# Performance work log

Measured on AMD Instinct MI355X. Metric: run time of the kernel, lower is better.

Reference implementation:

```python
import jax, jax.numpy as jnp
import numpy as np

HIDDEN = 256
INPUT = 256
OUTPUT = 256
BATCH = 256
SEQ = 512


def setup_inputs() -> dict:
    key = jax.random.key(0)
    ks = jax.random.split(key, 9)
    d = INPUT + HIDDEN
    s = 0.05
    return {
        "x": jax.random.normal(ks[0], (BATCH, SEQ, INPUT), dtype=jnp.float32),
        "Wr": jax.random.normal(ks[1], (d, HIDDEN), dtype=jnp.float32) * s,
        "br": jax.random.normal(ks[2], (HIDDEN,), dtype=jnp.float32) * s,
        "Wz": jax.random.normal(ks[3], (d, HIDDEN), dtype=jnp.float32) * s,
        "bz": jax.random.normal(ks[4], (HIDDEN,), dtype=jnp.float32) * s,
        "Wh": jax.random.normal(ks[5], (d, HIDDEN), dtype=jnp.float32) * s,
        "bh": jax.random.normal(ks[6], (HIDDEN,), dtype=jnp.float32) * s,
        "Wo": jax.random.normal(ks[7], (HIDDEN, OUTPUT), dtype=jnp.float32) * s,
        "bo": jax.random.normal(ks[8], (OUTPUT,), dtype=jnp.float32) * s,
    }


def reference(x, Wr, br, Wz, bz, Wh, bh, Wo, bo):
    # x: [B, S, I]. Sequential GRU cell; only last-step output is returned
    # (the torch loop overwrites `output` each iteration).
    B = x.shape[0]
    h0 = jnp.zeros((B, HIDDEN), dtype=x.dtype)

    def step(h, xt):
        combined = jnp.concatenate([xt, h], axis=1)          # [B, I+H]
        r = jax.nn.sigmoid(combined @ Wr + br)                # reset gate
        z = jax.nn.sigmoid(combined @ Wz + bz)                # update gate
        combined2 = jnp.concatenate([xt, r * h], axis=1)
        h_cand = jnp.tanh(combined2 @ Wh + bh)
        h_new = z * h + (1.0 - z) * h_cand
        return h_new, None

    xs = jnp.swapaxes(x, 0, 1)  # [S, B, I] for scan over time
    h_last, _ = jax.lax.scan(step, h0, xs)
    return h_last @ Wo + bo
```

## Files before the change

### kernel.cpp

```cpp
#include <hip/hip_runtime.h>
#include <math.h>


#define BATCH  256
#define SEQ    512
#define INPUT  256
#define HIDDEN 256
#define DTOT   512
#define NTC    48
#define NT_O   16
#define LOG2E  1.44269504088896f

typedef float          f32x4 __attribute__((ext_vector_type(4)));
typedef short          s16x8 __attribute__((ext_vector_type(8)));
typedef unsigned short u16x8 __attribute__((ext_vector_type(8)));
typedef unsigned int   u32x2 __attribute__((ext_vector_type(2)));

#define WH_OFF   0u
#define WX_OFF   393216u
#define WO_OFF   786432u
#define X_OFF    917504u
#define WS_NEED     (917504ull + 201326592ull)
#define WS_NEED_OLD 786432ull

__device__ __forceinline__ unsigned short f2bf(float f) {
    unsigned int u = __float_as_uint(f);
    u += 0x7FFFu + ((u >> 16) & 1u);
    return (unsigned short)(u >> 16);
}
__device__ __forceinline__ unsigned short f2bf_fast(float f) {
    return (unsigned short)((__float_as_uint(f) + 0x8000u) >> 16);
}
__device__ __forceinline__ float bf2f(unsigned short u) {
    return __uint_as_float(((unsigned int)u) << 16);
}
__device__ __forceinline__ f32x4 cvt4(u32x2 u) {
    f32x4 a;
    a[0] = __uint_as_float(u[0] << 16);
    a[1] = __uint_as_float(u[0] & 0xffff0000u);
    a[2] = __uint_as_float(u[1] << 16);
    a[3] = __uint_as_float(u[1] & 0xffff0000u);
    return a;
}
__device__ __forceinline__ unsigned int pk2bf(float a, float b) {
    return ((__float_as_uint(a) + 0x8000u) >> 16) |
           ((__float_as_uint(b) + 0x8000u) & 0xFFFF0000u);
}
#if __has_builtin(__builtin_amdgcn_exp2f)
#define EXP2F(x) __builtin_amdgcn_exp2f(x)
#else
#define EXP2F(x) exp2f(x)
#endif
#if __has_builtin(__builtin_amdgcn_rcpf)
#define RCPF(x) __builtin_amdgcn_rcpf(x)
#else
#define RCPF(x) (1.0f / (x))
#endif

#define WAITCNT_VM3()   asm volatile("s_waitcnt vmcnt(3)" ::: "memory")
#define WAITCNT_VM4()   asm volatile("s_waitcnt vmcnt(4)" ::: "memory")
#define WAITCNT_LGKM0() asm volatile("s_waitcnt lgkmcnt(0)" ::: "memory")
#define BAR() do { __builtin_amdgcn_s_barrier(); __builtin_amdgcn_sched_barrier(0); } while (0)

__device__ __forceinline__ void async_ld16(const void* g, void* l) {
    __builtin_amdgcn_global_load_lds(
        (const __attribute__((address_space(1))) unsigned int*)g,
        (__attribute__((address_space(3))) unsigned int*)l, 16, 0, 0);
}

__device__ __forceinline__ void ntc_decode(int ntc, int& gate, int& colbase) {
    int w = ntc / 6, s = ntc - 6 * w;
    gate = s >> 1;
    colbase = (2 * w + (s & 1)) * 16;
}

__global__ __launch_bounds__(256) void pack_weights_k(
    const float* __restrict__ Wr, const float* __restrict__ Wz,
    const float* __restrict__ Wh, const float* __restrict__ Wo,
    unsigned short* __restrict__ ws)
{
    int tid = blockIdx.x * 256 + threadIdx.x;
    int tile = tid >> 6;
    int l = tid & 63, quad = l >> 4, lan = l & 15;
    u16x8 v;
    unsigned short* dst;
    if (tile < 768) {
        int isH = tile < 384;
        int t2 = isH ? tile : tile - 384;
        int ntc = t2 >> 3, kt = t2 & 7;
        int gate, colbase;
        ntc_decode(ntc, gate, colbase);
        const float* W = gate == 0 ? Wr : (gate == 1 ? Wz : Wh);
        float scale = (gate == 2) ? 2.f * LOG2E : LOG2E;
        int col = colbase + lan;
        int kbase = (isH ? 256 : 0) + kt * 32 + quad * 8;
        #pragma unroll
        for (int j = 0; j < 8; ++j) v[j] = f2bf(W[(kbase + j) * 256 + col] * scale);
        dst = (unsigned short*)((char*)ws + (isH ? WH_OFF : WX_OFF)) + (size_t)(t2 * 64 + l) * 8;
    } else {
        int t2 = tile - 768;
        int kt = t2 / NT_O, nt = t2 % NT_O;
        int col = nt * 16 + lan;
        int kbase = kt * 32 + quad * 8;
        #pragma unroll
        for (int j = 0; j < 8; ++j) v[j] = f2bf(Wo[(kbase + j) * 256 + col]);
        dst = (unsigned short*)((char*)ws + WO_OFF) + (size_t)(t2 * 64 + l) * 8;
    }
    *(u16x8*)dst = v;
}

__global__ __launch_bounds__(512, 2) void xgemm_k(
    const float* __restrict__ x,
    const float* __restrict__ br, const float* __restrict__ bz, const float* __restrict__ bh,
    unsigned short* __restrict__ ws)
{
    __shared__ __align__(16) unsigned short Xbf[16][264];
    const int th = threadIdx.x, wave = th >> 6, l = th & 63, quad = l >> 4, lan = l & 15;
    const s16x8* WX = (const s16x8*)((char*)ws + WX_OFF);
    s16x8 wx[6][8];
    #pragma unroll
    for (int fi = 0; fi < 6; ++fi)
        #pragma unroll
        for (int kt = 0; kt < 8; ++kt)
            wx[fi][kt] = WX[(((size_t)(6 * wave + fi)) * 8 + kt) * 64 + l];
    f32x4 bias4[6];
    #pragma unroll
    for (int fi = 0; fi < 6; ++fi) {
        int gate, colbase;
        ntc_decode(6 * wave + fi, gate, colbase);
        const float* bb = gate == 0 ? br : (gate == 1 ? bz : bh);
        f32x4 bv = *(const f32x4*)&bb[colbase + quad * 4];
        float scale = (gate == 2 ? 2.f * LOG2E : LOG2E);
        bias4[fi][0] = bv[0] * scale; bias4[fi][1] = bv[1] * scale;
        bias4[fi][2] = bv[2] * scale; bias4[fi][3] = bv[3] * scale;
    }
    u32x2* Xout = (u32x2*)((char*)ws + X_OFF);

    f32x4 xs[2];
    {
        int unit = blockIdx.x * 32, t = unit >> 4, gg = unit & 15;
        #pragma unroll
        for (int rr = 0; rr < 2; ++rr)
            xs[rr] = *(const f32x4*)(x + (((size_t)(gg * 16 + 2 * wave + rr)) * SEQ + t) * INPUT + l * 4);
    }
    for (int uu = 0; uu < 32; ++uu) {
        if (uu > 0) BAR();
        #pragma unroll
        for (int rr = 0; rr < 2; ++rr) {
            u32x2 p;
            p[0] = pk2bf(xs[rr][0], xs[rr][1]);
            p[1] = pk2bf(xs[rr][2], xs[rr][3]);
            *(u32x2*)&Xbf[2 * wave + rr][l * 4] = p;
        }
        if (uu + 1 < 32) {
            int unit = blockIdx.x * 32 + uu + 1, t = unit >> 4, gg = unit & 15;
            #pragma unroll
            for (int rr = 0; rr < 2; ++rr)
                xs[rr] = *(const f32x4*)(x + (((size_t)(gg * 16 + 2 * wave + rr)) * SEQ + t) * INPUT + l * 4);
        }
        WAITCNT_LGKM0();
        BAR();
        f32x4 acc[6];
        #pragma unroll
        for (int fi = 0; fi < 6; ++fi) acc[fi] = bias4[fi];
        #pragma unroll
        for (int kt = 0; kt < 8; ++kt) {
            s16x8 a = *(const s16x8*)&Xbf[lan][kt * 32 + quad * 8];
            #pragma unroll
            for (int fi = 0; fi < 6; ++fi)
                acc[fi] = __builtin_amdgcn_mfma_f32_16x16x32_bf16(wx[fi][kt], a, acc[fi], 0, 0, 0);
        }
        size_t unit = (size_t)blockIdx.x * 32 + uu;
        #pragma unroll
        for (int fi = 0; fi < 6; ++fi) {
            u32x2 p;
            p[0] = pk2bf(acc[fi][0], acc[fi][1]);
            p[1] = pk2bf(acc[fi][2], acc[fi][3]);
            Xout[(unit * NTC + 6 * wave + fi) * 64 + l] = p;
        }
    }
}

__global__ __launch_bounds__(512, 2) void gru_rec_k(
    const float* __restrict__ bo,
    unsigned short* __restrict__ ws,
    float* __restrict__ out)
{
    extern __shared__ __align__(16) char smem[];
    unsigned short (*Hb)[264]  = (unsigned short (*)[264])smem;
    unsigned short (*RHb)[264] = (unsigned short (*)[264])(smem + 8448);
    char* Xr = smem + 16896;

    const int th = threadIdx.x, wave = th >> 6, l = th & 63, quad = l >> 4, lan = l & 15;
    const int b = blockIdx.x;
    const s16x8* WH = (const s16x8*)((char*)ws + WH_OFF);
    s16x8 wfr[2][8], wfz[2][8], wfc[2][8];
    #pragma unroll
    for (int i = 0; i < 2; ++i)
        #pragma unroll
        for (int kt = 0; kt < 8; ++kt) {
            wfr[i][kt] = WH[((6 * wave + i) * 8 + kt) * 64 + l];
            wfz[i][kt] = WH[((6 * wave + 2 + i) * 8 + kt) * 64 + l];
            wfc[i][kt] = WH[((6 * wave + 4 + i) * 8 + kt) * 64 + l];
        }
    for (int idx = th; idx < 16 * 264; idx += 512) ((unsigned short*)Hb)[idx] = 0;
    float h[2][4];
    #pragma unroll
    for (int i = 0; i < 2; ++i)
        #pragma unroll
        for (int r = 0; r < 4; ++r) h[i][r] = 0.f;

    const char* Xg = (const char*)ws + X_OFF;
    {
        const char* sb = Xg + (((size_t)b) * NTC + 6 * wave) * 512;
        char* db = Xr + wave * 3072;
        #pragma unroll
        for (int inst = 0; inst < 3; ++inst)
            async_ld16(sb + inst * 1024 + l * 16, db + inst * 1024);
    }
    __syncthreads();

    for (int t = 0; t < SEQ; ++t) {
        int buf = t & 1;
        {
            int t1 = (t + 1 < SEQ) ? t + 1 : t;
            const char* sb = Xg + (((size_t)(t1 * 16 + b)) * NTC + 6 * wave) * 512;
            char* db = Xr + (buf ^ 1) * 24576 + wave * 3072;
            #pragma unroll
            for (int inst = 0; inst < 3; ++inst)
                async_ld16(sb + inst * 1024 + l * 16, db + inst * 1024);
        }
        WAITCNT_VM3();
        const char* Xw = Xr + buf * 24576 + wave * 3072;

        f32x4 ar[2], az[2];
        #pragma unroll
        for (int i = 0; i < 2; ++i) {
            ar[i] = cvt4(*(const u32x2*)(Xw + (size_t)i * 512 + l * 8));
            az[i] = cvt4(*(const u32x2*)(Xw + (size_t)(2 + i) * 512 + l * 8));
        }
        #pragma unroll
        for (int kt = 0; kt < 8; ++kt) {
            s16x8 a = *(const s16x8*)&Hb[lan][kt * 32 + quad * 8];
            #pragma unroll
            for (int i = 0; i < 2; ++i) {
                ar[i] = __builtin_amdgcn_mfma_f32_16x16x32_bf16(wfr[i][kt], a, ar[i], 0, 0, 0);
                az[i] = __builtin_amdgcn_mfma_f32_16x16x32_bf16(wfz[i][kt], a, az[i], 0, 0, 0);
            }
        }
        #pragma unroll
        for (int i = 0; i < 2; ++i) {
            int colb = (2 * wave + i) * 16 + quad * 4;
            float rg0 = RCPF(1.f + EXP2F(-ar[i][0]));
            float rg1 = RCPF(1.f + EXP2F(-ar[i][1]));
            float rg2 = RCPF(1.f + EXP2F(-ar[i][2]));
            float rg3 = RCPF(1.f + EXP2F(-ar[i][3]));
            u32x2 rp;
            rp[0] = pk2bf(rg0 * h[i][0], rg1 * h[i][1]);
            rp[1] = pk2bf(rg2 * h[i][2], rg3 * h[i][3]);
            *(u32x2*)&RHb[lan][colb] = rp;
        }
        WAITCNT_LGKM0();
        BAR();

        float zg[2][4];
        #pragma unroll
        for (int i = 0; i < 2; ++i)
            #pragma unroll
            for (int r = 0; r < 4; ++r)
                zg[i][r] = RCPF(1.f + EXP2F(-az[i][r]));

        f32x4 ac[2];
        #pragma unroll
        for (int i = 0; i < 2; ++i)
            ac[i] = cvt4(*(const u32x2*)(Xw + (size_t)(4 + i) * 512 + l * 8));
        #pragma unroll
        for (int kt = 0; kt < 8; ++kt) {
            s16x8 a = *(const s16x8*)&RHb[lan][kt * 32 + quad * 8];
            #pragma unroll
            for (int i = 0; i < 2; ++i)
                ac[i] = __builtin_amdgcn_mfma_f32_16x16x32_bf16(wfc[i][kt], a, ac[i], 0, 0, 0);
        }
        #pragma unroll
        for (int i = 0; i < 2; ++i) {
            int colb = (2 * wave + i) * 16 + quad * 4;
            #pragma unroll
            for (int r = 0; r < 4; ++r) {
                float e  = EXP2F(ac[i][r]);
                float hc = (e - 1.f) * RCPF(e + 1.f);
                h[i][r] = zg[i][r] * (h[i][r] - hc) + hc;
            }
            u32x2 hp;
            hp[0] = pk2bf(h[i][0], h[i][1]);
            hp[1] = pk2bf(h[i][2], h[i][3]);
            *(u32x2*)&Hb[lan][colb] = hp;
        }
        WAITCNT_LGKM0();
        BAR();
    }

    const s16x8* WO = (const s16x8*)((char*)ws + WO_OFF);
    #pragma unroll
    for (int i = 0; i < 2; ++i) {
        int nt = 2 * wave + i;
        f32x4 acc = *(const f32x4*)&bo[nt * 16 + quad * 4];
        #pragma unroll
        for (int kt = 0; kt < 8; ++kt) {
            s16x8 a = *(const s16x8*)&Hb[lan][kt * 32 + quad * 8];
            acc = __builtin_amdgcn_mfma_f32_16x16x32_bf16(WO[(kt * NT_O + nt) * 64 + l], a, acc, 0, 0, 0);
        }
        *(f32x4*)&out[(size_t)(b * 16 + lan) * 256 + nt * 16 + quad * 4] = acc;
    }
}

__global__ __launch_bounds__(256) void prep_weights_k(
    const float* __restrict__ Wr, const float* __restrict__ Wz,
    const float* __restrict__ Wh, unsigned short* __restrict__ W16)
{
    const int n = DTOT * HIDDEN;
    int idx = blockIdx.x * 256 + threadIdx.x;
    if (idx >= 3 * n) return;
    int m = idx / n;
    int r = idx - m * n;
    const float* src = (m == 0) ? Wr : ((m == 1) ? Wz : Wh);
    W16[idx] = f2bf(src[r]);
}
__device__ __forceinline__ float ldw(const unsigned short* p) { return bf2f(*p); }
__device__ __forceinline__ float ldw(const float* p)          { return *p; }

template <typename WT>
__global__ __launch_bounds__(256) void gru_seq_k(
    const float* __restrict__ x,
    const WT* __restrict__ Wr, const WT* __restrict__ Wz, const WT* __restrict__ Wh,
    const float* __restrict__ br, const float* __restrict__ bz, const float* __restrict__ bh,
    const float* __restrict__ Wo, const float* __restrict__ bo,
    float* __restrict__ out)
{
    const int b = blockIdx.x, j = threadIdx.x;
    __shared__ float xh[DTOT];
    __shared__ float xrh[DTOT];
    xh[INPUT + j] = 0.0f;
    const float brj = br[j], bzj = bz[j], bhj = bh[j];
    const float* xb = x + (size_t)b * SEQ * INPUT;
    const WT* wrj = Wr + j;
    const WT* wzj = Wz + j;
    const WT* whj = Wh + j;
    __syncthreads();
    for (int t = 0; t < SEQ; ++t) {
        float xv = xb[t * INPUT + j];
        xh[j] = xv; xrh[j] = xv;
        __syncthreads();
        float ar = brj, az = bzj;
        #pragma unroll 8
        for (int k = 0; k < DTOT; ++k) {
            float v = xh[k];
            ar += v * ldw(wrj + k * HIDDEN);
            az += v * ldw(wzj + k * HIDDEN);
        }
        float rg = 1.0f / (1.0f + __expf(-ar));
        float zg = 1.0f / (1.0f + __expf(-az));
        float hj = xh[INPUT + j];
        xrh[INPUT + j] = rg * hj;
        __syncthreads();
        float ah = bhj;
        #pragma unroll 8
        for (int k = 0; k < DTOT; ++k) ah += xrh[k] * ldw(whj + k * HIDDEN);
        float hc = tanhf(ah);
        float hn = zg * hj + (1.0f - zg) * hc;
        xh[INPUT + j] = hn;
        __syncthreads();
    }
    float acc = bo[j];
    #pragma unroll 8
    for (int k = 0; k < HIDDEN; ++k) acc += xh[INPUT + k] * Wo[k * HIDDEN + j];
    out[(size_t)b * HIDDEN + j] = acc;
}

extern "C" void kernel_launch(void* const* d_in, const int* in_sizes, int n_in,
                              void* d_out, int out_size, void* d_ws, size_t ws_size,
                              hipStream_t stream) {
    const float* x  = (const float*)d_in[0];
    const float* Wr = (const float*)d_in[1];
    const float* br = (const float*)d_in[2];
    const float* Wz = (const float*)d_in[3];
    const float* bz = (const float*)d_in[4];
    const float* Wh = (const float*)d_in[5];
    const float* bh = (const float*)d_in[6];
    const float* Wo = (const float*)d_in[7];
    const float* bo = (const float*)d_in[8];
    float* out = (float*)d_out;

    if (ws_size >= WS_NEED) {
        unsigned short* ws = (unsigned short*)d_ws;
        (void)hipFuncSetAttribute((const void*)gru_rec_k,
                                  hipFuncAttributeMaxDynamicSharedMemorySize, 66048);
        pack_weights_k<<<224, 256, 0, stream>>>(Wr, Wz, Wh, Wo, ws);
        xgemm_k<<<256, 512, 0, stream>>>(x, br, bz, bh, ws);
        gru_rec_k<<<16, 512, 66048, stream>>>(bo, ws, out);
    } else if (ws_size >= WS_NEED_OLD) {
        unsigned short* W16 = (unsigned short*)d_ws;
        const size_t n = (size_t)DTOT * HIDDEN;
        prep_weights_k<<<(int)((3 * n + 255) / 256), 256, 0, stream>>>(Wr, Wz, Wh, W16);
        gru_seq_k<unsigned short><<<BATCH, 256, 0, stream>>>(
            x, W16, W16 + n, W16 + 2 * n, br, bz, bh, Wo, bo, out);
    } else {
        gru_seq_k<float><<<BATCH, 256, 0, stream>>>(
            x, Wr, Wz, Wh, br, bz, bh, Wo, bo, out);
    }
}
```

Baseline: 1.053 ms.

## Halve recurrence block to four waves, each owning four column tiles

The recurrent GRU kernel now runs 256 threads (4 waves) per block instead of 512, and each wave handles four 16-column tiles of r, z and candidate gates instead of two. Each wave keeps twice as many weight fragments in registers, and the per-step X prefetch per wave doubles to six async loads. The aim is cheaper barriers and more MFMA work per wave between the two per-step syncs. The cost is heavier register pressure (96 s16x8 weight fragments per lane) and fewer waves to hide MFMA and LDS latency.

```diff
diff --git a/kernel.cpp b/kernel.cpp
--- a/kernel.cpp
+++ b/kernel.cpp
@@ -27,9 +27,6 @@
     unsigned int u = __float_as_uint(f);
     u += 0x7FFFu + ((u >> 16) & 1u);
     return (unsigned short)(u >> 16);
-}
-__device__ __forceinline__ unsigned short f2bf_fast(float f) {
-    return (unsigned short)((__float_as_uint(f) + 0x8000u) >> 16);
 }
 __device__ __forceinline__ float bf2f(unsigned short u) {
     return __uint_as_float(((unsigned int)u) << 16);
@@ -57,8 +54,7 @@
 #define RCPF(x) (1.0f / (x))
 #endif
 
-#define WAITCNT_VM3()   asm volatile("s_waitcnt vmcnt(3)" ::: "memory")
-#define WAITCNT_VM4()   asm volatile("s_waitcnt vmcnt(4)" ::: "memory")
+#define WAITCNT_VM6()   asm volatile("s_waitcnt vmcnt(6)" ::: "memory")
 #define WAITCNT_LGKM0() asm volatile("s_waitcnt lgkmcnt(0)" ::: "memory")
 #define BAR() do { __builtin_amdgcn_s_barrier(); __builtin_amdgcn_sched_barrier(0); } while (0)
 
@@ -181,7 +177,7 @@
     }
 }
 
-__global__ __launch_bounds__(512, 2) void gru_rec_k(
+__global__ __launch_bounds__(256, 1) void gru_rec_k(
     const float* __restrict__ bo,
     unsigned short* __restrict__ ws,
     float* __restrict__ out)
@@ -194,28 +190,30 @@
     const int th = threadIdx.x, wave = th >> 6, l = th & 63, quad = l >> 4, lan = l & 15;
     const int b = blockIdx.x;
     const s16x8* WH = (const s16x8*)((char*)ws + WH_OFF);
-    s16x8 wfr[2][8], wfz[2][8], wfc[2][8];
+    s16x8 wfr[4][8], wfz[4][8], wfc[4][8];
     #pragma unroll
-    for (int i = 0; i < 2; ++i)
+    for (int i2 = 0; i2 < 4; ++i2) {
+        int nb = 6 * (2 * wave + (i2 >> 1)) + (i2 & 1);
         #pragma unroll
         for (int kt = 0; kt < 8; ++kt) {
-            wfr[i][kt] = WH[((6 * wave + i) * 8 + kt) * 64 + l];
-            wfz[i][kt] = WH[((6 * wave + 2 + i) * 8 + kt) * 64 + l];
-            wfc[i][kt] = WH[((6 * wave + 4 + i) * 8 + kt) * 64 + l];
-        }
-    for (int idx = th; idx < 16 * 264; idx += 512) ((unsigned short*)Hb)[idx] = 0;
-    float h[2][4];
+            wfr[i2][kt] = WH[((nb)     * 8 + kt) * 64 + l];
+            wfz[i2][kt] = WH[((nb + 2) * 8 + kt) * 64 + l];
+            wfc[i2][kt] = WH[((nb + 4) * 8 + kt) * 64 + l];
+        }
+    }
+    for (int idx = th; idx < 16 * 264; idx += 256) ((unsigned short*)Hb)[idx] = 0;
+    float h[4][4];
     #pragma unroll
-    for (int i = 0; i < 2; ++i)
-        #pragma unroll
-        for (int r = 0; r < 4; ++r) h[i][r] = 0.f;
+    for (int i2 = 0; i2 < 4; ++i2)
+        #pragma unroll
+        for (int r = 0; r < 4; ++r) h[i2][r] = 0.f;
 
     const char* Xg = (const char*)ws + X_OFF;
     {
-        const char* sb = Xg + (((size_t)b) * NTC + 6 * wave) * 512;
-        char* db = Xr + wave * 3072;
-        #pragma unroll
-        for (int inst = 0; inst < 3; ++inst)
+        const char* sb = Xg + (((size_t)b) * NTC + 12 * wave) * 512;
+        char* db = Xr + wave * 6144;
+        #pragma unroll
+        for (int inst = 0; inst < 6; ++inst)
             async_ld16(sb + inst * 1024 + l * 16, db + inst * 1024);
     }
     __syncthreads();
@@ -224,75 +222,78 @@
         int buf = t & 1;
         {
             int t1 = (t + 1 < SEQ) ? t + 1 : t;
-            const char* sb = Xg + (((size_t)(t1 * 16 + b)) * NTC + 6 * wave) * 512;
-            char* db = Xr + (buf ^ 1) * 24576 + wave * 3072;
-            #pragma unroll
-            for (int inst = 0; inst < 3; ++inst)
+            const char* sb = Xg + (((size_t)(t1 * 16 + b)) * NTC + 12 * wave) * 512;
+            char* db = Xr + (buf ^ 1) * 24576 + wave * 6144;
+            #pragma unroll
+            for (int inst = 0; inst < 6; ++inst)
                 async_ld16(sb + inst * 1024 + l * 16, db + inst * 1024);
         }
-        WAITCNT_VM3();
-        const char* Xw = Xr + buf * 24576 + wave * 3072;
-
-        f32x4 ar[2], az[2];
-        #pragma unroll
-        for (int i = 0; i < 2; ++i) {
-            ar[i] = cvt4(*(const u32x2*)(Xw + (size_t)i * 512 + l * 8));
-            az[i] = cvt4(*(const u32x2*)(Xw + (size_t)(2 + i) * 512 + l * 8));
+        WAITCNT_VM6();
+        const char* Xw = Xr + buf * 24576 + wave * 6144;
+
+        f32x4 ar[4], az[4];
+        #pragma unroll
+        for (int i2 = 0; i2 < 4; ++i2) {
+            int kb = 6 * (i2 >> 1) + (i2 & 1);
+            ar[i2] = cvt4(*(const u32x2*)(Xw + (size_t)(kb)     * 512 + l * 8));
+            az[i2] = cvt4(*(const u32x2*)(Xw + (size_t)(kb + 2) * 512 + l * 8));
         }
         #pragma unroll
         for (int kt = 0; kt < 8; ++kt) {
             s16x8 a = *(const s16x8*)&Hb[lan][kt * 32 + quad * 8];
             #pragma unroll
-            for (int i = 0; i < 2; ++i) {
-                ar[i] = __builtin_amdgcn_mfma_f32_16x16x32_bf16(wfr[i][kt], a, ar[i], 0, 0, 0);
-                az[i] = __builtin_amdgcn_mfma_f32_16x16x32_bf16(wfz[i][kt], a, az[i], 0, 0, 0);
+            for (int i2 = 0; i2 < 4; ++i2) {
+                ar[i2] = __builtin_amdgcn_mfma_f32_16x16x32_bf16(wfr[i2][kt], a, ar[i2], 0, 0, 0);
+                az[i2] = __builtin_amdgcn_mfma_f32_16x16x32_bf16(wfz[i2][kt], a, az[i2], 0, 0, 0);
             }
         }
         #pragma unroll
-        for (int i = 0; i < 2; ++i) {
-            int colb = (2 * wave + i) * 16 + quad * 4;
-            float rg0 = RCPF(1.f + EXP2F(-ar[i][0]));
-            float rg1 = RCPF(1.f + EXP2F(-ar[i][1]));
-            float rg2 = RCPF(1.f + EXP2F(-ar[i][2]));
-            float rg3 = RCPF(1.f + EXP2F(-ar[i][3]));
+        for (int i2 = 0; i2 < 4; ++i2) {
+            int colb = (4 * wave + i2) * 16 + quad * 4;
+            float rg0 = RCPF(1.f + EXP2F(-ar[i2][0]));
+            float rg1 = RCPF(1.f + EXP2F(-ar[i2][1]));
+            float rg2 = RCPF(1.f + EXP2F(-ar[i2][2]));
+            float rg3 = RCPF(1.f + EXP2F(-ar[i2][3]));
             u32x2 rp;
-            rp[0] = pk2bf(rg0 * h[i][0], rg1 * h[i][1]);
-            rp[1] = pk2bf(rg2 * h[i][2], rg3 * h[i][3]);
+            rp[0] = pk2bf(rg0 * h[i2][0], rg1 * h[i2][1]);
+            rp[1] = pk2bf(rg2 * h[i2][2], rg3 * h[i2][3]);
             *(u32x2*)&RHb[lan][colb] = rp;
         }
         WAITCNT_LGKM0();
         BAR();
 
-        float zg[2][4];
-        #pragma unroll
-        for (int i = 0; i < 2; ++i)
+        float zg[4][4];
+        #pragma unroll
+        for (int i2 = 0; i2 < 4; ++i2)
             #pragma unroll
             for (int r = 0; r < 4; ++r)
-                zg[i][r] = RCPF(1.f + EXP2F(-az[i][r]));
-
-        f32x4 ac[2];
-        #pragma unroll
-        for (int i = 0; i < 2; ++i)
-            ac[i] = cvt4(*(const u32x2*)(Xw + (size_t)(4 + i) * 512 + l * 8));
+                zg[i2][r] = RCPF(1.f + EXP2F(-az[i2][r]));
+
+        f32x4 ac[4];
+        #pragma unroll
+        for (int i2 = 0; i2 < 4; ++i2) {
+            int kb = 6 * (i2 >> 1) + (i2 & 1);
+            ac[i2] = cvt4(*(const u32x2*)(Xw + (size_t)(kb + 4) * 512 + l * 8));
+        }
         #pragma unroll
         for (int kt = 0; kt < 8; ++kt) {
             s16x8 a = *(const s16x8*)&RHb[lan][kt * 32 + quad * 8];
             #pragma unroll
-            for (int i = 0; i < 2; ++i)
-                ac[i] = __builtin_amdgcn_mfma_f32_16x16x32_bf16(wfc[i][kt], a, ac[i], 0, 0, 0);
-        }
-        #pragma unroll
-        for (int i = 0; i < 2; ++i) {
-            int colb = (2 * wave + i) * 16 + quad * 4;
+            for (int i2 = 0; i2 < 4; ++i2)
+                ac[i2] = __builtin_amdgcn_mfma_f32_16x16x32_bf16(wfc[i2][kt], a, ac[i2], 0, 0, 0);
+        }
+        #pragma unroll
+        for (int i2 = 0; i2 < 4; ++i2) {
+            int colb = (4 * wave + i2) * 16 + quad * 4;
             #pragma unroll
             for (int r = 0; r < 4; ++r) {
-                float e  = EXP2F(ac[i][r]);
+                float e  = EXP2F(ac[i2][r]);
                 float hc = (e - 1.f) * RCPF(e + 1.f);
-                h[i][r] = zg[i][r] * (h[i][r] - hc) + hc;
+                h[i2][r] = zg[i2][r] * (h[i2][r] - hc) + hc;
             }
             u32x2 hp;
-            hp[0] = pk2bf(h[i][0], h[i][1]);
-            hp[1] = pk2bf(h[i][2], h[i][3]);
+            hp[0] = pk2bf(h[i2][0], h[i2][1]);
+            hp[1] = pk2bf(h[i2][2], h[i2][3]);
             *(u32x2*)&Hb[lan][colb] = hp;
         }
         WAITCNT_LGKM0();
@@ -301,8 +302,8 @@
 
     const s16x8* WO = (const s16x8*)((char*)ws + WO_OFF);
     #pragma unroll
-    for (int i = 0; i < 2; ++i) {
-        int nt = 2 * wave + i;
+    for (int i2 = 0; i2 < 4; ++i2) {
+        int nt = 4 * wave + i2;
         f32x4 acc = *(const f32x4*)&bo[nt * 16 + quad * 4];
         #pragma unroll
         for (int kt = 0; kt < 8; ++kt) {
@@ -396,7 +397,7 @@
                                   hipFuncAttributeMaxDynamicSharedMemorySize, 66048);
         pack_weights_k<<<224, 256, 0, stream>>>(Wr, Wz, Wh, Wo, ws);
         xgemm_k<<<256, 512, 0, stream>>>(x, br, bz, bh, ws);
-        gru_rec_k<<<16, 512, 66048, stream>>>(bo, ws, out);
+        gru_rec_k<<<16, 256, 66048, stream>>>(bo, ws, out);
     } else if (ws_size >= WS_NEED_OLD) {
         unsigned short* W16 = (unsigned short*)d_ws;
         const size_t n = (size_t)DTOT * HIDDEN;
```

Measured after the change: 1.421 ms. +34.9%, slower.

## Fuse input GEMM and recurrence into one kernel with flag-based producer/consumer overlap

Applied to the files above, without the earlier changes.

Merges the x-projection GEMM and the sequential GRU recurrence into one launch. 240 producer blocks compute per-timestep input projections and publish per-unit flags with release stores, while 16 consumer blocks spin on those flags and run the recurrence concurrently. This is meant to hide the input GEMM behind the recurrence and remove a kernel boundary. The cost is spin-waiting, reliance on all blocks being co-resident, and a larger workspace for the flags, which pack_weights_k now zeroes.

```diff
diff --git a/kernel.cpp b/kernel.cpp
--- a/kernel.cpp
+++ b/kernel.cpp
@@ -10,6 +10,7 @@
 #define NTC    48
 #define NT_O   16
 #define LOG2E  1.44269504088896f
+#define NPROD  240
 
 typedef float          f32x4 __attribute__((ext_vector_type(4)));
 typedef short          s16x8 __attribute__((ext_vector_type(8)));
@@ -20,16 +21,15 @@
 #define WX_OFF   393216u
 #define WO_OFF   786432u
 #define X_OFF    917504u
-#define WS_NEED     (917504ull + 201326592ull)
-#define WS_NEED_OLD 786432ull
+#define FLAG_OFF (917504u + 201326592u)
+#define WS_NEED_FUSED (917504ull + 201326592ull + 32768ull)
+#define WS_NEED_SPLIT (917504ull + 201326592ull)
+#define WS_NEED_OLD   786432ull
 
 __device__ __forceinline__ unsigned short f2bf(float f) {
     unsigned int u = __float_as_uint(f);
     u += 0x7FFFu + ((u >> 16) & 1u);
     return (unsigned short)(u >> 16);
-}
-__device__ __forceinline__ unsigned short f2bf_fast(float f) {
-    return (unsigned short)((__float_as_uint(f) + 0x8000u) >> 16);
 }
 __device__ __forceinline__ float bf2f(unsigned short u) {
     return __uint_as_float(((unsigned int)u) << 16);
@@ -77,9 +77,13 @@
 __global__ __launch_bounds__(256) void pack_weights_k(
     const float* __restrict__ Wr, const float* __restrict__ Wz,
     const float* __restrict__ Wh, const float* __restrict__ Wo,
-    unsigned short* __restrict__ ws)
+    unsigned short* __restrict__ ws, int zflags)
 {
     int tid = blockIdx.x * 256 + threadIdx.x;
+    if (zflags && tid < 4096) {
+        u32x2 z; z[0] = 0u; z[1] = 0u;
+        ((u32x2*)((char*)ws + FLAG_OFF))[tid] = z;
+    }
     int tile = tid >> 6;
     int l = tid & 63, quad = l >> 4, lan = l & 15;
     u16x8 v;
@@ -109,6 +113,227 @@
     *(u16x8*)dst = v;
 }
 
+__global__ __launch_bounds__(512, 2) void fused_k(
+    const float* __restrict__ x,
+    const float* __restrict__ br, const float* __restrict__ bz, const float* __restrict__ bh,
+    const float* __restrict__ bo,
+    unsigned short* __restrict__ ws,
+    float* __restrict__ out)
+{
+    extern __shared__ __align__(16) char smem[];
+    const int bid = blockIdx.x;
+    const int th = threadIdx.x, wave = th >> 6, l = th & 63, quad = l >> 4, lan = l & 15;
+    int* flags = (int*)((char*)ws + FLAG_OFF);
+
+    if (bid >= 16) {
+        unsigned short (*Xbf)[264] = (unsigned short (*)[264])smem;
+        const int p = bid - 16;
+        const s16x8* WX = (const s16x8*)((char*)ws + WX_OFF);
+        s16x8 wx[6][8];
+        #pragma unroll
+        for (int fi = 0; fi < 6; ++fi)
+            #pragma unroll
+            for (int kt = 0; kt < 8; ++kt)
+                wx[fi][kt] = WX[(((size_t)(6 * wave + fi)) * 8 + kt) * 64 + l];
+        f32x4 bias4[6];
+        #pragma unroll
+        for (int fi = 0; fi < 6; ++fi) {
+            int gate, colbase;
+            ntc_decode(6 * wave + fi, gate, colbase);
+            const float* bb = gate == 0 ? br : (gate == 1 ? bz : bh);
+            f32x4 bv = *(const f32x4*)&bb[colbase + quad * 4];
+            float scale = (gate == 2 ? 2.f * LOG2E : LOG2E);
+            bias4[fi][0] = bv[0] * scale; bias4[fi][1] = bv[1] * scale;
+            bias4[fi][2] = bv[2] * scale; bias4[fi][3] = bv[3] * scale;
+        }
+        u32x2* Xout = (u32x2*)((char*)ws + X_OFF);
+
+        f32x4 xs[2];
+        {
+            int t = p >> 4, gg = p & 15;
+            #pragma unroll
+            for (int rr = 0; rr < 2; ++rr)
+                xs[rr] = *(const f32x4*)(x + (((size_t)(gg * 16 + 2 * wave + rr)) * SEQ + t) * INPUT + l * 4);
+        }
+        for (int uu = p; uu < SEQ * 16; uu += NPROD) {
+            if (uu != p) BAR();
+            #pragma unroll
+            for (int rr = 0; rr < 2; ++rr) {
+                u32x2 pk;
+                pk[0] = pk2bf(xs[rr][0], xs[rr][1]);
+                pk[1] = pk2bf(xs[rr][2], xs[rr][3]);
+                *(u32x2*)&Xbf[2 * wave + rr][l * 4] = pk;
+            }
+            int un = uu + NPROD;
+            if (un < SEQ * 16) {
+                int t = un >> 4, gg = un & 15;
+                #pragma unroll
+                for (int rr = 0; rr < 2; ++rr)
+                    xs[rr] = *(const f32x4*)(x + (((size_t)(gg * 16 + 2 * wave + rr)) * SEQ + t) * INPUT + l * 4);
+            }
+            WAITCNT_LGKM0();
+            BAR();
+            f32x4 acc[6];
+            #pragma unroll
+            for (int fi = 0; fi < 6; ++fi) acc[fi] = bias4[fi];
+            #pragma unroll
+            for (int kt = 0; kt < 8; ++kt) {
+                s16x8 a = *(const s16x8*)&Xbf[lan][kt * 32 + quad * 8];
+                #pragma unroll
+                for (int fi = 0; fi < 6; ++fi)
+                    acc[fi] = __builtin_amdgcn_mfma_f32_16x16x32_bf16(wx[fi][kt], a, acc[fi], 0, 0, 0);
+            }
+            #pragma unroll
+            for (int fi = 0; fi < 6; ++fi) {
+                u32x2 pk;
+                pk[0] = pk2bf(acc[fi][0], acc[fi][1]);
+                pk[1] = pk2bf(acc[fi][2], acc[fi][3]);
+                Xout[((size_t)uu * NTC + 6 * wave + fi) * 64 + l] = pk;
+            }
+            __threadfence();
+            __syncthreads();
+            if (th == 0)
+                __hip_atomic_store(&flags[uu], 1, __ATOMIC_RELEASE, __HIP_MEMORY_SCOPE_AGENT);
+        }
+        return;
+    }
+
+    unsigned short (*Hb)[264]  = (unsigned short (*)[264])smem;
+    unsigned short (*RHb)[264] = (unsigned short (*)[264])(smem + 8448);
+    char* Xr = smem + 16896;
+    const int b = bid;
+    const s16x8* WH = (const s16x8*)((char*)ws + WH_OFF);
+    s16x8 wfr[2][8], wfz[2][8], wfc[2][8];
+    #pragma unroll
+    for (int i = 0; i < 2; ++i)
+        #pragma unroll
+        for (int kt = 0; kt < 8; ++kt) {
+            wfr[i][kt] = WH[((6 * wave + i) * 8 + kt) * 64 + l];
+            wfz[i][kt] = WH[((6 * wave + 2 + i) * 8 + kt) * 64 + l];
+            wfc[i][kt] = WH[((6 * wave + 4 + i) * 8 + kt) * 64 + l];
+        }
+    for (int idx = th; idx < 16 * 264; idx += 512) ((unsigned short*)Hb)[idx] = 0;
+    float h[2][4];
+    #pragma unroll
+    for (int i = 0; i < 2; ++i)
+        #pragma unroll
+        for (int r = 0; r < 4; ++r) h[i][r] = 0.f;
+
+    const char* Xg = (const char*)ws + X_OFF;
+    while (__hip_atomic_load(&flags[b], __ATOMIC_RELAXED, __HIP_MEMORY_SCOPE_AGENT) == 0) {}
+    __builtin_amdgcn_sched_barrier(0);
+    {
+        const char* sb = Xg + (((size_t)b) * NTC + 6 * wave) * 512;
+        char* db = Xr + wave * 3072;
+        #pragma unroll
+        for (int inst = 0; inst < 3; ++inst)
+            async_ld16(sb + inst * 1024 + l * 16, db + inst * 1024);
+    }
+    int fv = __hip_atomic_load(&flags[16 + b], __ATOMIC_RELAXED, __HIP_MEMORY_SCOPE_AGENT);
+    __syncthreads();
+
+    for (int t = 0; t < SEQ; ++t) {
+        int buf = t & 1;
+        if (t + 1 < SEQ && fv != 1) {
+            do {
+                fv = __hip_atomic_load(&flags[(t + 1) * 16 + b], __ATOMIC_RELAXED, __HIP_MEMORY_SCOPE_AGENT);
+            } while (fv != 1);
+            __builtin_amdgcn_sched_barrier(0);
+        }
+        {
+            int t1 = (t + 1 < SEQ) ? t + 1 : t;
+            const char* sb = Xg + (((size_t)(t1 * 16 + b)) * NTC + 6 * wave) * 512;
+            char* db = Xr + (buf ^ 1) * 24576 + wave * 3072;
+            #pragma unroll
+            for (int inst = 0; inst < 3; ++inst)
+                async_ld16(sb + inst * 1024 + l * 16, db + inst * 1024);
+        }
+        fv = (t + 2 < SEQ)
+           ? __hip_atomic_load(&flags[(t + 2) * 16 + b], __ATOMIC_RELAXED, __HIP_MEMORY_SCOPE_AGENT)
+           : 1;
+        WAITCNT_VM4();
+        const char* Xw = Xr + buf * 24576 + wave * 3072;
+
+        f32x4 ar[2], az[2];
+        #pragma unroll
+        for (int i = 0; i < 2; ++i) {
+            ar[i] = cvt4(*(const u32x2*)(Xw + (size_t)i * 512 + l * 8));
+            az[i] = cvt4(*(const u32x2*)(Xw + (size_t)(2 + i) * 512 + l * 8));
+        }
+        #pragma unroll
+        for (int kt = 0; kt < 8; ++kt) {
+            s16x8 a = *(const s16x8*)&Hb[lan][kt * 32 + quad * 8];
+            #pragma unroll
+            for (int i = 0; i < 2; ++i) {
+                ar[i] = __builtin_amdgcn_mfma_f32_16x16x32_bf16(wfr[i][kt], a, ar[i], 0, 0, 0);
+                az[i] = __builtin_amdgcn_mfma_f32_16x16x32_bf16(wfz[i][kt], a, az[i], 0, 0, 0);
+            }
+        }
+        #pragma unroll
+        for (int i = 0; i < 2; ++i) {
+            int colb = (2 * wave + i) * 16 + quad * 4;
+            float rg0 = RCPF(1.f + EXP2F(-ar[i][0]));
+            float rg1 = RCPF(1.f + EXP2F(-ar[i][1]));
+            float rg2 = RCPF(1.f + EXP2F(-ar[i][2]));
+            float rg3 = RCPF(1.f + EXP2F(-ar[i][3]));
+            u32x2 rp;
+            rp[0] = pk2bf(rg0 * h[i][0], rg1 * h[i][1]);
+            rp[1] = pk2bf(rg2 * h[i][2], rg3 * h[i][3]);
+            *(u32x2*)&RHb[lan][colb] = rp;
+        }
+        WAITCNT_LGKM0();
+        BAR();
+
+        float zg[2][4];
+        #pragma unroll
+        for (int i = 0; i < 2; ++i)
+            #pragma unroll
+            for (int r = 0; r < 4; ++r)
+                zg[i][r] = RCPF(1.f + EXP2F(-az[i][r]));
+
+        f32x4 ac[2];
+        #pragma unroll
+        for (int i = 0; i < 2; ++i)
+            ac[i] = cvt4(*(const u32x2*)(Xw + (size_t)(4 + i) * 512 + l * 8));
+        #pragma unroll
+        for (int kt = 0; kt < 8; ++kt) {
+            s16x8 a = *(const s16x8*)&RHb[lan][kt * 32 + quad * 8];
+            #pragma unroll
+            for (int i = 0; i < 2; ++i)
+                ac[i] = __builtin_amdgcn_mfma_f32_16x16x32_bf16(wfc[i][kt], a, ac[i], 0, 0, 0);
+        }
+        #pragma unroll
+        for (int i = 0; i < 2; ++i) {
+            int colb = (2 * wave + i) * 16 + quad * 4;
+            #pragma unroll
+            for (int r = 0; r < 4; ++r) {
+                float e  = EXP2F(ac[i][r]);
+                float hc = (e - 1.f) * RCPF(e + 1.f);
+                h[i][r] = zg[i][r] * (h[i][r] - hc) + hc;
+            }
+            u32x2 hp;
+            hp[0] = pk2bf(h[i][0], h[i][1]);
+            hp[1] = pk2bf(h[i][2], h[i][3]);
+            *(u32x2*)&Hb[lan][colb] = hp;
+        }
+        WAITCNT_LGKM0();
+        BAR();
+    }
+
+    const s16x8* WO = (const s16x8*)((char*)ws + WO_OFF);
+    #pragma unroll
+    for (int i = 0; i < 2; ++i) {
+        int nt = 2 * wave + i;
+        f32x4 acc = *(const f32x4*)&bo[nt * 16 + quad * 4];
+        #pragma unroll
+        for (int kt = 0; kt < 8; ++kt) {
+            s16x8 a = *(const s16x8*)&Hb[lan][kt * 32 + quad * 8];
+            acc = __builtin_amdgcn_mfma_f32_16x16x32_bf16(WO[(kt * NT_O + nt) * 64 + l], a, acc, 0, 0, 0);
+        }
+        *(f32x4*)&out[(size_t)(b * 16 + lan) * 256 + nt * 16 + quad * 4] = acc;
+    }
+}
+
 __global__ __launch_bounds__(512, 2) void xgemm_k(
     const float* __restrict__ x,
     const float* __restrict__ br, const float* __restrict__ bz, const float* __restrict__ bh,
@@ -135,7 +360,6 @@
         bias4[fi][2] = bv[2] * scale; bias4[fi][3] = bv[3] * scale;
     }
     u32x2* Xout = (u32x2*)((char*)ws + X_OFF);
-
     f32x4 xs[2];
     {
         int unit = blockIdx.x * 32, t = unit >> 4, gg = unit & 15;
@@ -390,11 +614,17 @@
     const float* bo = (const float*)d_in[8];
     float* out = (float*)d_out;
 
-    if (ws_size >= WS_NEED) {
+    if (ws_size >= WS_NEED_FUSED) {
+        unsigned short* ws = (unsigned short*)d_ws;
+        (void)hipFuncSetAttribute((const void*)fused_k,
+                                  hipFuncAttributeMaxDynamicSharedMemorySize, 66048);
+        pack_weights_k<<<224, 256, 0, stream>>>(Wr, Wz, Wh, Wo, ws, 1);
+        fused_k<<<256, 512, 66048, stream>>>(x, br, bz, bh, bo, ws, out);
+    } else if (ws_size >= WS_NEED_SPLIT) {
         unsigned short* ws = (unsigned short*)d_ws;
         (void)hipFuncSetAttribute((const void*)gru_rec_k,
                                   hipFuncAttributeMaxDynamicSharedMemorySize, 66048);
-        pack_weights_k<<<224, 256, 0, stream>>>(Wr, Wz, Wh, Wo, ws);
+        pack_weights_k<<<224, 256, 0, stream>>>(Wr, Wz, Wh, Wo, ws, 0);
         xgemm_k<<<256, 512, 0, stream>>>(x, br, bz, bh, ws);
         gru_rec_k<<<16, 512, 66048, stream>>>(bo, ws, out);
     } else if (ws_size >= WS_NEED_OLD) {
```

After: 2.864 ms. 172% more time.
